# Kernel optimization log

Measured on AMD Instinct MI355X. Metric: run time of the kernel, lower is better.

Reference implementation:

```python
import jax, jax.numpy as jnp
import numpy as np

BIG_NEGATIVE_SCALAR = -10000.0
SEGMENT_SIZE = 64
DILATION = 2
D_K = 128
POS_EMB_SCALING = 1.0


def setup_inputs() -> dict:
    key = jax.random.key(0)
    k1, k2, k3, k4, k5 = jax.random.split(key, 5)
    B, T, E = 4, 8192, 1024
    d_k, d_v = 128, 128
    inv = 1.0 / np.sqrt(d_k)
    return {
        "x_in": jax.random.normal(k1, (B, T, E), dtype=jnp.float32),
        "P": jax.random.normal(k2, (T, T), dtype=jnp.float32),
        "Wk": jax.random.normal(k3, (d_k, E), dtype=jnp.float32) * inv,
        "Wq": jax.random.normal(k4, (d_k, E), dtype=jnp.float32) * inv,
        "Wv": jax.random.normal(k5, (d_v, E), dtype=jnp.float32) * inv,
    }


def reference(x_in, P, Wk, Wq, Wv):
    B, T, E = x_in.shape
    seg, dil = SEGMENT_SIZE, DILATION
    nseg = T // seg
    norm_fact = 1.0 / np.sqrt(D_K)
    d_v = Wv.shape[0]

    # [B, nseg, seg, E] -> [B, seg, E, nseg], then dilate along the segment axis
    x_view = x_in.reshape(B, nseg, seg, E).transpose(0, 2, 3, 1)
    x_dil = x_view[:, :, :, ::dil]                      # [B, seg, E, nseg_d]

    Q = jnp.einsum('ijkl,mk->ijlm', x_dil, Wq)          # [B, seg, nseg_d, d_k]
    K = jnp.einsum('ijkl,mk->ijlm', x_dil, Wk)
    V = jnp.einsum('ijkl,mk->ijlm', x_dil, Wv)          # [B, seg, nseg_d, d_v]

    KQ = jnp.einsum('ijkp,ijop->ijko', K, Q)            # [B, seg, nseg_d(key), nseg_d(query)]

    causal_mask = jnp.tril(jnp.ones((nseg, nseg), dtype=bool))[::dil, ::dil]
    KQ = jnp.where(causal_mask, KQ, BIG_NEGATIVE_SCALAR)

    # positional bias: P is [T, T]; segment-level bias at within-segment offset 0
    Ps = P * POS_EMB_SCALING
    p_bias = Ps.reshape(nseg, seg, nseg, seg)[::dil, :, ::dil, :][:, 0, :, 0]
    KQ = KQ + p_bias

    smKQ = jax.nn.softmax(KQ * norm_fact, axis=2)       # softmax over key axis
    att = jnp.einsum('ijld,ijlm->ijdm', smKQ, V)        # [B, seg, nseg_d, d_v]

    # 'same' padding: scatter dilated outputs back into full-length sequence
    res = jnp.zeros((B, T, d_v), dtype=x_in.dtype)
    res = res.at[:, ::dil, :].set(att.reshape(B, -1, d_v))
    return res
```

## Files before the change

### kernel.cpp

```cpp
#include <hip/hip_runtime.h>

#define B_  4
#define T_  8192
#define E_  1024
#define DK_ 128

typedef __attribute__((ext_vector_type(8))) _Float16 half8;
typedef __attribute__((ext_vector_type(4))) float float4v;

__device__ __forceinline__ half8 cvt8h(float4 a, float4 b) {
    half8 r;
    r[0] = (_Float16)a.x; r[1] = (_Float16)a.y; r[2] = (_Float16)a.z; r[3] = (_Float16)a.w;
    r[4] = (_Float16)b.x; r[5] = (_Float16)b.y; r[6] = (_Float16)b.z; r[7] = (_Float16)b.w;
    return r;
}

__global__ void wconv(const float* __restrict__ Wk, const float* __restrict__ Wq,
                      const float* __restrict__ Wv, ushort* __restrict__ W16) {
    const int g   = blockIdx.x * 256 + threadIdx.x;
    const int c   = g & 7;
    const int ki  = (g >> 3) & 15;
    const int row = g >> 7;
    const float* src = (row < 128) ? (Wq + (size_t)row * E_)
                     : (row < 256) ? (Wk + (size_t)(row - 128) * E_)
                                   : (Wv + (size_t)(row - 256) * E_);
    src += ki * 64 + c * 8;
    *(half8*)(W16 + (size_t)(ki * 384 + row) * 64 + c * 8) =
        cvt8h(*(const float4*)src, *(const float4*)(src + 4));
}

__global__ __launch_bounds__(512, 2)
void dilattn(const float* __restrict__ x_in, const float* __restrict__ P,
             const ushort* __restrict__ W16, float* __restrict__ out)
{
    __shared__ __align__(16) ushort sh[2 * 64 * 72 + 2 * 384 * 72];
    ushort* xs0   = sh;
    ushort* ws0   = sh + 2 * 64 * 72;
    float*  lds_f = (float*)sh;
    constexpr int A_OFF = 0;
    constexpr int B_OFF = 8192;
    constexpr int S_OFF = 8192;
    const float NORMF = 0.08838834764831845f;

    const int tid  = threadIdx.x;
    const int lane = tid & 63;
    const int w    = __builtin_amdgcn_readfirstlane(tid >> 6);
    const int b    = blockIdx.x >> 6;
    const int s    = blockIdx.x & 63;

    const int lr   = lane & 15;
    const int lg   = lane >> 4;
    const int mt   = w & 3;
    const int half = w >> 2;

    const int c8 = tid & 7;
    const int xr = tid >> 3;
    const float*  xrow  = x_in + ((size_t)b * T_ + 128 * xr + s) * E_ + c8 * 8;
    const ushort* wbase = W16 + xr * 64 + c8 * 8;

    float4v acc[12];
#pragma unroll
    for (int j = 0; j < 12; ++j) acc[j] = (float4v){0.f, 0.f, 0.f, 0.f};

    uint4  wr[2][6];
    float4 xa[2][2];

#define ISSUE_STAGE(K, SL) { \
    _Pragma("unroll") \
    for (int p = 0; p < 6; ++p) wr[SL][p] = *(const uint4*)(wbase + (K) * 24576 + p * 4096); \
    xa[SL][0] = *(const float4*)(xrow + (K) * 64); \
    xa[SL][1] = *(const float4*)(xrow + (K) * 64 + 4); }

#define WRITE_STAGE(K, SL) { \
    const int wb_ = ((K) & 1) * (384 * 72); \
    _Pragma("unroll") \
    for (int p = 0; p < 6; ++p) *(uint4*)&ws0[wb_ + (xr + 64 * p) * 72 + c8 * 8] = wr[SL][p]; \
    *(half8*)&xs0[((K) & 1) * (64 * 72) + xr * 72 + c8 * 8] = cvt8h(xa[SL][0], xa[SL][1]); }

    ISSUE_STAGE(0, 0);
    ISSUE_STAGE(1, 1);
    WRITE_STAGE(0, 0);
    __syncthreads();

#pragma unroll
    for (int k = 0; k < 16; ++k) {
        if (k < 14) ISSUE_STAGE(k + 2, k & 1);
        if (k < 15) WRITE_STAGE(k + 1, (k + 1) & 1);
        const int xb = (k & 1) * (64 * 72);
        const int wb = (k & 1) * (384 * 72);
#pragma unroll
        for (int kk = 0; kk < 2; ++kk) {
            const half8 afr = *(const half8*)&xs0[xb + (mt * 16 + lr) * 72 + kk * 32 + lg * 8];
#pragma unroll
            for (int j = 0; j < 12; ++j) {
                const half8 bfr = *(const half8*)&ws0[wb + ((half * 12 + j) * 16 + lr) * 72 + kk * 32 + lg * 8];
                acc[j] = __builtin_amdgcn_mfma_f32_16x16x32_f16(afr, bfr, acc[j], 0, 0, 0);
            }
        }
        __syncthreads();
    }

    const int rbase = mt * 16 + lg * 4;
#pragma unroll
    for (int j = 0; j < 12; ++j) {
        const int nt = half * 12 + j;
        const int n  = nt * 16 + lr;
        if (nt < 8) {
#pragma unroll
            for (int r = 0; r < 4; ++r) {
                const int l = rbase + r;
                lds_f[A_OFF + l * 128 + ((n + 4 * l) & 127)] = acc[j][r];
            }
        } else if (nt < 16) {
            const int m = n - 128;
#pragma unroll
            for (int r = 0; r < 4; ++r) {
                const int l = rbase + r;
                lds_f[B_OFF + m * 64 + ((l + m) & 63)] = acc[j][r];
            }
        }
    }
    __syncthreads();

    float pb[8];
#pragma unroll
    for (int i = 0; i < 8; ++i)
        pb[i] = P[(size_t)lane * ((size_t)128 * T_) + (size_t)(w * 8 + i) * 128];

    float sd[8];
#pragma unroll
    for (int i = 0; i < 8; ++i) sd[i] = 0.f;

    for (int m4 = 0; m4 < 32; ++m4) {
        const int mm = 4 * m4;
        const float k0 = lds_f[B_OFF + (mm + 0) * 64 + ((lane + mm + 0) & 63)];
        const float k1 = lds_f[B_OFF + (mm + 1) * 64 + ((lane + mm + 1) & 63)];
        const float k2 = lds_f[B_OFF + (mm + 2) * 64 + ((lane + mm + 2) & 63)];
        const float k3 = lds_f[B_OFF + (mm + 3) * 64 + ((lane + mm + 3) & 63)];
#pragma unroll
        for (int i = 0; i < 8; ++i) {
            const int q = w * 8 + i;
            const float4 qv = *(const float4*)&lds_f[A_OFF + q * 128 + ((4 * (m4 + q)) & 127)];
            sd[i] = fmaf(k0, qv.x, fmaf(k1, qv.y, fmaf(k2, qv.z, fmaf(k3, qv.w, sd[i]))));
        }
    }
    __syncthreads();

    if (half == 1) {
#pragma unroll
        for (int j = 4; j < 12; ++j) {
            const int nt = 12 + j;
            const int m  = nt * 16 + lr - 256;
#pragma unroll
            for (int r = 0; r < 4; ++r) {
                const int l = rbase + r;
                lds_f[A_OFF + l * 128 + ((m + 4 * l) & 127)] = acc[j][r];
            }
        }
    }

#pragma unroll
    for (int i = 0; i < 8; ++i) {
        const int q = w * 8 + i;
        const float logit = ((lane >= q ? sd[i] : -10000.f) + pb[i]) * NORMF;
        float mx = logit;
#pragma unroll
        for (int off = 32; off >= 1; off >>= 1) mx = fmaxf(mx, __shfl_xor(mx, off));
        const float ev = __expf(logit - mx);
        float sum = ev;
#pragma unroll
        for (int off = 32; off >= 1; off >>= 1) sum += __shfl_xor(sum, off);
        lds_f[S_OFF + lane * 65 + q] = ev * (1.0f / sum);
    }
    __syncthreads();

    float4 o0 = {0,0,0,0}, o1 = {0,0,0,0}, o2 = {0,0,0,0}, o3 = {0,0,0,0};
    for (int k = 0; k < 64; ++k) {
        const float p = lds_f[S_OFF + k * 65 + lane];
        const int base = A_OFF + k * 128;
        const float4 v0 = *(const float4*)&lds_f[base + ((16 * w + 0  + 4 * k) & 127)];
        const float4 v1 = *(const float4*)&lds_f[base + ((16 * w + 4  + 4 * k) & 127)];
        const float4 v2 = *(const float4*)&lds_f[base + ((16 * w + 8  + 4 * k) & 127)];
        const float4 v3 = *(const float4*)&lds_f[base + ((16 * w + 12 + 4 * k) & 127)];
        o0.x = fmaf(p, v0.x, o0.x); o0.y = fmaf(p, v0.y, o0.y); o0.z = fmaf(p, v0.z, o0.z); o0.w = fmaf(p, v0.w, o0.w);
        o1.x = fmaf(p, v1.x, o1.x); o1.y = fmaf(p, v1.y, o1.y); o1.z = fmaf(p, v1.z, o1.z); o1.w = fmaf(p, v1.w, o1.w);
        o2.x = fmaf(p, v2.x, o2.x); o2.y = fmaf(p, v2.y, o2.y); o2.z = fmaf(p, v2.z, o2.z); o2.w = fmaf(p, v2.w, o2.w);
        o3.x = fmaf(p, v3.x, o3.x); o3.y = fmaf(p, v3.y, o3.y); o3.z = fmaf(p, v3.z, o3.z); o3.w = fmaf(p, v3.w, o3.w);
    }
    float* orow = out + ((size_t)b * T_ + (size_t)(2 * (s * 64 + lane))) * DK_ + w * 16;
    *(float4*)(orow + 0)  = o0;
    *(float4*)(orow + 4)  = o1;
    *(float4*)(orow + 8)  = o2;
    *(float4*)(orow + 12) = o3;
    const float4 z = {0.f, 0.f, 0.f, 0.f};
    *(float4*)(orow + DK_ + 0)  = z;
    *(float4*)(orow + DK_ + 4)  = z;
    *(float4*)(orow + DK_ + 8)  = z;
    *(float4*)(orow + DK_ + 12) = z;
}

extern "C" void kernel_launch(void* const* d_in, const int* in_sizes, int n_in,
                              void* d_out, int out_size, void* d_ws, size_t ws_size,
                              hipStream_t stream) {
    (void)in_sizes; (void)n_in; (void)out_size; (void)ws_size;
    const float* x_in = (const float*)d_in[0];
    const float* P    = (const float*)d_in[1];
    const float* Wk   = (const float*)d_in[2];
    const float* Wq   = (const float*)d_in[3];
    const float* Wv   = (const float*)d_in[4];
    float* out = (float*)d_out;
    ushort* W16 = (ushort*)d_ws;

    wconv<<<dim3(192), dim3(256), 0, stream>>>(Wk, Wq, Wv, W16);
    dilattn<<<dim3(256), dim3(512), 0, stream>>>(x_in, P, W16, out);
}
```

Baseline: 468.4 us.

## Single-buffer LDS staging for projection GEMM and zero output via memset

Replaces the two-deep double-buffered LDS pipeline for the x/W projection with a single LDS buffer plus one register prefetch stage, with barriers before and after each LDS write. This shrinks the LDS footprint, which could let more blocks stay resident. The zeroing of odd output rows moves from the kernel into a hipMemsetAsync over the whole output before launch. The cost is less load/compute overlap, an extra barrier per k-step, and a full extra pass writing the output buffer.

```diff
diff --git a/kernel.cpp b/kernel.cpp
--- a/kernel.cpp
+++ b/kernel.cpp
@@ -33,10 +33,9 @@
 void dilattn(const float* __restrict__ x_in, const float* __restrict__ P,
              const ushort* __restrict__ W16, float* __restrict__ out)
 {
-    __shared__ __align__(16) ushort sh[2 * 64 * 72 + 2 * 384 * 72];
-    ushort* xs0   = sh;
-    ushort* ws0   = sh + 2 * 64 * 72;
-    float*  lds_f = (float*)sh;
+    __shared__ float lds_f[16384];
+    ushort* xs  = (ushort*)lds_f;
+    ushort* wsm = xs + 64 * 72;
     constexpr int A_OFF = 0;
     constexpr int B_OFF = 8192;
     constexpr int S_OFF = 8192;
@@ -55,50 +54,49 @@
 
     const int c8 = tid & 7;
     const int xr = tid >> 3;
-    const float*  xrow  = x_in + ((size_t)b * T_ + 128 * xr + s) * E_ + c8 * 8;
-    const ushort* wbase = W16 + xr * 64 + c8 * 8;
+    const float*  xrow = x_in + ((size_t)b * T_ + 128 * xr + s) * E_ + c8 * 8;
+    const ushort* wrow = W16 + xr * 64 + c8 * 8;
 
     float4v acc[12];
 #pragma unroll
     for (int j = 0; j < 12; ++j) acc[j] = (float4v){0.f, 0.f, 0.f, 0.f};
 
-    uint4  wr[2][6];
-    float4 xa[2][2];
-
-#define ISSUE_STAGE(K, SL) { \
-    _Pragma("unroll") \
-    for (int p = 0; p < 6; ++p) wr[SL][p] = *(const uint4*)(wbase + (K) * 24576 + p * 4096); \
-    xa[SL][0] = *(const float4*)(xrow + (K) * 64); \
-    xa[SL][1] = *(const float4*)(xrow + (K) * 64 + 4); }
-
-#define WRITE_STAGE(K, SL) { \
-    const int wb_ = ((K) & 1) * (384 * 72); \
-    _Pragma("unroll") \
-    for (int p = 0; p < 6; ++p) *(uint4*)&ws0[wb_ + (xr + 64 * p) * 72 + c8 * 8] = wr[SL][p]; \
-    *(half8*)&xs0[((K) & 1) * (64 * 72) + xr * 72 + c8 * 8] = cvt8h(xa[SL][0], xa[SL][1]); }
-
-    ISSUE_STAGE(0, 0);
-    ISSUE_STAGE(1, 1);
-    WRITE_STAGE(0, 0);
-    __syncthreads();
-
-#pragma unroll
-    for (int k = 0; k < 16; ++k) {
-        if (k < 14) ISSUE_STAGE(k + 2, k & 1);
-        if (k < 15) WRITE_STAGE(k + 1, (k + 1) & 1);
-        const int xb = (k & 1) * (64 * 72);
-        const int wb = (k & 1) * (384 * 72);
+    float4 xa0, xa1;
+    uint4  wa[6];
+    xa0 = *(const float4*)(xrow);
+    xa1 = *(const float4*)(xrow + 4);
+#pragma unroll
+    for (int p = 0; p < 6; ++p) wa[p] = *(const uint4*)(wrow + p * 4096);
+
+    for (int ki = 0; ki < 16; ++ki) {
+        __syncthreads();
+        *(half8*)&xs[xr * 72 + c8 * 8] = cvt8h(xa0, xa1);
+#pragma unroll
+        for (int p = 0; p < 6; ++p)
+            *(uint4*)&wsm[(xr + 64 * p) * 72 + c8 * 8] = wa[p];
+        __syncthreads();
+
+        if (ki < 15) {
+            const int k0 = (ki + 1) * 64;
+            xa0 = *(const float4*)(xrow + k0);
+            xa1 = *(const float4*)(xrow + k0 + 4);
+            const int wk = (ki + 1) * 24576;
+#pragma unroll
+            for (int p = 0; p < 6; ++p)
+                wa[p] = *(const uint4*)(wrow + wk + p * 4096);
+        }
+
 #pragma unroll
         for (int kk = 0; kk < 2; ++kk) {
-            const half8 afr = *(const half8*)&xs0[xb + (mt * 16 + lr) * 72 + kk * 32 + lg * 8];
+            const half8 afr = *(const half8*)&xs[(mt * 16 + lr) * 72 + kk * 32 + lg * 8];
 #pragma unroll
             for (int j = 0; j < 12; ++j) {
-                const half8 bfr = *(const half8*)&ws0[wb + ((half * 12 + j) * 16 + lr) * 72 + kk * 32 + lg * 8];
+                const half8 bfr = *(const half8*)&wsm[((half * 12 + j) * 16 + lr) * 72 + kk * 32 + lg * 8];
                 acc[j] = __builtin_amdgcn_mfma_f32_16x16x32_f16(afr, bfr, acc[j], 0, 0, 0);
             }
         }
-        __syncthreads();
-    }
+    }
+    __syncthreads();
 
     const int rbase = mt * 16 + lg * 4;
 #pragma unroll
@@ -192,17 +190,12 @@
     *(float4*)(orow + 4)  = o1;
     *(float4*)(orow + 8)  = o2;
     *(float4*)(orow + 12) = o3;
-    const float4 z = {0.f, 0.f, 0.f, 0.f};
-    *(float4*)(orow + DK_ + 0)  = z;
-    *(float4*)(orow + DK_ + 4)  = z;
-    *(float4*)(orow + DK_ + 8)  = z;
-    *(float4*)(orow + DK_ + 12) = z;
 }
 
 extern "C" void kernel_launch(void* const* d_in, const int* in_sizes, int n_in,
                               void* d_out, int out_size, void* d_ws, size_t ws_size,
                               hipStream_t stream) {
-    (void)in_sizes; (void)n_in; (void)out_size; (void)ws_size;
+    (void)in_sizes; (void)n_in; (void)ws_size;
     const float* x_in = (const float*)d_in[0];
     const float* P    = (const float*)d_in[1];
     const float* Wk   = (const float*)d_in[2];
@@ -211,6 +204,7 @@
     float* out = (float*)d_out;
     ushort* W16 = (ushort*)d_ws;
 
+    hipMemsetAsync(d_out, 0, (size_t)out_size * sizeof(float), stream);
     wconv<<<dim3(192), dim3(256), 0, stream>>>(Wk, Wq, Wv, W16);
     dilattn<<<dim3(256), dim3(512), 0, stream>>>(x_in, P, W16, out);
 }
```

New measurement: 468.1 us. No clear change (-0.1%).
